# Performance work log

Measured on AMD Instinct MI355X. Metric: run time of the kernel, lower is better.

The kernel has to match this reference:

```python
import jax, jax.numpy as jnp
import numpy as np

N = 100000   # nodes
D = 128      # embedding_dim
E = 1600000  # edges
L = 3        # num_layers


def setup_inputs() -> dict:
    key = jax.random.key(0)
    ks = jax.random.split(key, 10)
    s = 1.0 / np.sqrt(D)
    def w(k, shape):
        return jax.random.uniform(k, shape, jnp.float32, -s, s)
    return {
        "x": jax.random.normal(ks[0], (N, D), jnp.float32),
        "edge_index": jax.random.randint(ks[1], (2, E), 0, N, jnp.int32),
        "Wp": w(ks[2], (L - 1, D, D)),   # project Linear weight (per layer)
        "bp": w(ks[3], (L - 1, D)),      # project Linear bias
        "Wl": w(ks[4], (L - 1, D, D)),   # lin_l (aggregated neighbors)
        "bl": w(ks[5], (L - 1, D)),
        "Wr": w(ks[6], (L - 1, D, D)),   # lin_r (root, no bias)
        "Wl_out": w(ks[7], (D, D)),
        "bl_out": w(ks[8], (D,)),
        "Wr_out": w(ks[9], (D, D)),
    }


def _sage(x, src, dst, inv_deg, Wl, bl, Wr, Wp=None, bp=None, normalize=False):
    # PyG SAGEConv: project applies to messages only; root term uses original x.
    h = jax.nn.relu(x @ Wp.T + bp) if Wp is not None else x
    agg = jax.ops.segment_sum(h[src], dst, num_segments=N) * inv_deg  # mean aggr
    out = agg @ Wl.T + bl + x @ Wr.T
    if normalize:
        out = out / jnp.maximum(
            jnp.linalg.norm(out, axis=-1, keepdims=True), 1e-12)
    return out


def reference(x, edge_index, Wp, bp, Wl, bl, Wr, Wl_out, bl_out, Wr_out):
    src, dst = edge_index[0], edge_index[1]
    deg = jax.ops.segment_sum(jnp.ones((src.shape[0],), x.dtype), dst,
                              num_segments=N)
    inv_deg = (1.0 / jnp.maximum(deg, 1.0))[:, None]  # isolated nodes -> 0 agg
    for i in range(L - 1):
        x = jax.nn.relu(
            _sage(x, src, dst, inv_deg, Wl[i], bl[i], Wr[i], Wp[i], bp[i],
                  normalize=True))
    return _sage(x, src, dst, inv_deg, Wl_out, bl_out, Wr_out)
```

## Files before the change

kernel.cpp:

```cpp
#include <hip/hip_runtime.h>
#include <math.h>

#define D 128

typedef short s8v __attribute__((ext_vector_type(8)));
typedef float f32x4 __attribute__((ext_vector_type(4)));
typedef unsigned short u16x8 __attribute__((ext_vector_type(8)));

__device__ __forceinline__ unsigned short f2bf(float f) {
  union { float f; unsigned u; } c; c.f = f;
  unsigned u = c.u;
  unsigned r = (u + 0x7fffu + ((u >> 16) & 1u)) >> 16;
  return (unsigned short)r;
}

__device__ __forceinline__ void gload_lds16(const void* g, void* l) {
  __builtin_amdgcn_global_load_lds((const __attribute__((address_space(1))) void*)g,
                                   (__attribute__((address_space(3))) void*)l, 16, 0, 0);
}

__global__ __launch_bounds__(256) void k_prep(const float* __restrict__ Wp,
                                              const float* __restrict__ Wl,
                                              const float* __restrict__ Wr,
                                              const float* __restrict__ Wlo,
                                              const float* __restrict__ Wro,
                                              unsigned short* __restrict__ Wb,
                                              const int* __restrict__ dst,
                                              int* __restrict__ bucketCnt, int E_) {
  int t = threadIdx.x;
  if (blockIdx.x < 128) {
    int i = blockIdx.x * 256 + t;
    const float* s;
    int off;
    if (i < 8192)       { s = Wp;  off = 0; }
    else if (i < 16384) { s = Wl;  off = 8192; }
    else if (i < 24576) { s = Wr;  off = 16384; }
    else if (i < 28672) { s = Wlo; off = 24576; }
    else                { s = Wro; off = 28672; }
    float4 a = ((const float4*)s)[i - off];
    ushort4 o;
    o.x = f2bf(a.x); o.y = f2bf(a.y); o.z = f2bf(a.z); o.w = f2bf(a.w);
    ((ushort4*)Wb)[i] = o;
  } else {
    __shared__ int hist[512];
    hist[t] = 0; hist[t + 256] = 0;
    __syncthreads();
    int base = (blockIdx.x - 128) * 4096;
#pragma unroll
    for (int i = 0; i < 16; i++) {
      int e = base + i * 256 + t;
      if (e < E_) atomicAdd(&hist[dst[e] >> 8], 1);
    }
    __syncthreads();
    int c = hist[t];       if (c) atomicAdd(&bucketCnt[t], c);
    c = hist[t + 256];     if (c) atomicAdd(&bucketCnt[t + 256], c);
  }
}

__global__ __launch_bounds__(512) void k_bucket_scan(const int* __restrict__ cnt,
                                                     int* __restrict__ base,
                                                     int* __restrict__ cursor,
                                                     int* __restrict__ row_start,
                                                     int n, int E_) {
  __shared__ int bs[512];
  int t = threadIdx.x;
  int orig = cnt[t];
  bs[t] = orig;
  __syncthreads();
  for (int off = 1; off < 512; off <<= 1) {
    int x = (t >= off) ? bs[t - off] : 0;
    __syncthreads();
    bs[t] += x;
    __syncthreads();
  }
  int ex = bs[t] - orig;
  base[t] = ex;
  cursor[t] = ex;
  if (t == 511) base[512] = bs[511];
  if (t == 0) row_start[n] = E_;
}

__global__ __launch_bounds__(1024) void k_partA(const int* __restrict__ src,
                                                const int* __restrict__ dst,
                                                int* __restrict__ cursor,
                                                unsigned* __restrict__ pairs, int E_) {
  __shared__ int hist[512];
  __shared__ int gbase[512];
  int t = threadIdx.x;
  int base = blockIdx.x * 16384;
  if (t < 512) hist[t] = 0;
  __syncthreads();
  unsigned p_[16];
  int k_[16];
#pragma unroll
  for (int i = 0; i < 16; i++) {
    int e = base + i * 1024 + t;
    if (e < E_) {
      int s = src[e], d = dst[e];
      p_[i] = ((unsigned)s << 8) | (unsigned)(d & 255);
      k_[i] = d >> 8;
      atomicAdd(&hist[k_[i]], 1);
    } else {
      k_[i] = -1;
    }
  }
  __syncthreads();
  if (t < 512) {
    int c = hist[t];
    gbase[t] = c ? atomicAdd(&cursor[t], c) : 0;
    hist[t] = 0;
  }
  __syncthreads();
#pragma unroll
  for (int i = 0; i < 16; i++) {
    if (k_[i] >= 0) {
      int r = atomicAdd(&hist[k_[i]], 1);
      pairs[gbase[k_[i]] + r] = p_[i];
    }
  }
}

__global__ __launch_bounds__(256) void k_partB(const unsigned* __restrict__ pairs,
                                               const int* __restrict__ bucketBase,
                                               int* __restrict__ row_start,
                                               int* __restrict__ csr, int n) {
  __shared__ int cnt[256];
  __shared__ int scn[256];
  int k = blockIdx.x, t = threadIdx.x;
  int node0 = k << 8;
  int pbeg = bucketBase[k], pend = bucketBase[k + 1];
  cnt[t] = 0;
  __syncthreads();
  for (int p = pbeg + t; p < pend; p += 256) atomicAdd(&cnt[pairs[p] & 255], 1);
  __syncthreads();
  int c = cnt[t];
  scn[t] = c;
  __syncthreads();
  for (int off = 1; off < 256; off <<= 1) {
    int x = (t >= off) ? scn[t - off] : 0;
    __syncthreads();
    scn[t] += x;
    __syncthreads();
  }
  int ex = scn[t] - c;
  int node = node0 + t;
  if (node < n) row_start[node] = pbeg + ex;
  __syncthreads();
  cnt[t] = pbeg + ex;
  __syncthreads();
  for (int p = pbeg + t; p < pend; p += 256) {
    unsigned pr = pairs[p];
    int slot = atomicAdd(&cnt[pr & 255], 1);
    csr[slot] = (int)(pr >> 8);
  }
}

__global__ __launch_bounds__(256) void k_aggregate(const unsigned short* __restrict__ h,
                                                   unsigned short* __restrict__ agg,
                                                   const int* __restrict__ row_start,
                                                   const int* __restrict__ csr, int n) {
  int node = (blockIdx.x * 256 + threadIdx.x) >> 4;
  int li = threadIdx.x & 15;
  if (node >= n) return;
  int rs0 = row_start[node];
  int dc = row_start[node + 1] - rs0;
  const int* ce = csr + rs0;
  const char* base = (const char*)h + li * 16;

  float accL[4], accH[4];
#pragma unroll
  for (int q = 0; q < 4; q++) { accL[q] = 0.f; accH[q] = 0.f; }

#define ACCR(v)                                                        \
  {                                                                    \
    unsigned dw[4] = {(v).x, (v).y, (v).z, (v).w};                     \
    _Pragma("unroll") for (int q = 0; q < 4; q++) {                    \
      accL[q] += __uint_as_float(dw[q] << 16);                         \
      accH[q] += __uint_as_float(dw[q] & 0xffff0000u);                 \
    }                                                                  \
  }

  int e = 0;
  bool more = (3 < dc);
  int s0 = 0, s1 = 0, s2 = 0, s3 = 0;
  if (more) { s0 = ce[0]; s1 = ce[1]; s2 = ce[2]; s3 = ce[3]; }
  while (more) {
    uint4 v0 = *(const uint4*)(base + (size_t)s0 * 256);
    uint4 v1 = *(const uint4*)(base + (size_t)s1 * 256);
    uint4 v2 = *(const uint4*)(base + (size_t)s2 * 256);
    uint4 v3 = *(const uint4*)(base + (size_t)s3 * 256);
    e += 4;
    more = (e + 3 < dc);
    if (more) { s0 = ce[e]; s1 = ce[e + 1]; s2 = ce[e + 2]; s3 = ce[e + 3]; }
    ACCR(v0); ACCR(v1); ACCR(v2); ACCR(v3);
  }
  if (e < dc)     { uint4 v = *(const uint4*)(base + (size_t)ce[e] * 256);     ACCR(v); }
  if (e + 1 < dc) { uint4 v = *(const uint4*)(base + (size_t)ce[e + 1] * 256); ACCR(v); }
  if (e + 2 < dc) { uint4 v = *(const uint4*)(base + (size_t)ce[e + 2] * 256); ACCR(v); }
#undef ACCR

  float iv = 1.0f / (float)(dc > 0 ? dc : 1);
  u16x8 o;
#pragma unroll
  for (int q = 0; q < 4; q++) {
    o[2 * q] = f2bf(accL[q] * iv);
    o[2 * q + 1] = f2bf(accH[q] * iv);
  }
  *(u16x8*)(agg + (size_t)node * D + li * 8) = o;
}

__device__ __forceinline__ int swz_chunk(int r, int c) { return (r << 4) + (c ^ (r & 7)); }

template <int CVT>
__global__ __launch_bounds__(512, 4) void k_gemm_proj(const void* __restrict__ Av,
                                                      const unsigned short* __restrict__ W,
                                                      const float* __restrict__ bias,
                                                      unsigned short* __restrict__ out,
                                                      unsigned short* __restrict__ xb_out,
                                                      int n) {
  __shared__ __align__(16) unsigned short Wlds[128 * 128];
  int t = threadIdx.x;
  int wv = t >> 6, l = t & 63, lg = l >> 4, ln = l & 15;
  int rb = blockIdx.x * 128 + wv * 16;
  int arow = rb + ln;
  if (arow >= n) arow = n - 1;

  s8v a[4];
  if (CVT) {
    const float* Af = (const float*)Av + (size_t)arow * D + lg * 8;
#pragma unroll
    for (int ks = 0; ks < 4; ++ks) {
      float4 f0 = *(const float4*)(Af + ks * 32);
      float4 f1 = *(const float4*)(Af + ks * 32 + 4);
      s8v av;
      av[0] = (short)f2bf(f0.x); av[1] = (short)f2bf(f0.y);
      av[2] = (short)f2bf(f0.z); av[3] = (short)f2bf(f0.w);
      av[4] = (short)f2bf(f1.x); av[5] = (short)f2bf(f1.y);
      av[6] = (short)f2bf(f1.z); av[7] = (short)f2bf(f1.w);
      a[ks] = av;
      if (xb_out) *(s8v*)(xb_out + (size_t)arow * D + lg * 8 + ks * 32) = av;
    }
  } else {
    const s8v* Ap = (const s8v*)((const unsigned short*)Av + (size_t)arow * D + lg * 8);
#pragma unroll
    for (int ks = 0; ks < 4; ++ks) a[ks] = Ap[ks * 4];
  }

#pragma unroll
  for (int i = 0; i < 4; ++i) {
    int idx = t + i * 512;
    int r = idx >> 4, k = idx & 15;
    int c = k ^ (r & 7);
    gload_lds16(W + r * 128 + c * 8, &Wlds[idx * 8]);
  }
  __syncthreads();

  f32x4 acc[8];
#pragma unroll
  for (int f = 0; f < 8; ++f) acc[f] = (f32x4){0.f, 0.f, 0.f, 0.f};
#pragma unroll
  for (int ks = 0; ks < 4; ++ks) {
#pragma unroll
    for (int f = 0; f < 8; ++f) {
      s8v b = *(const s8v*)&Wlds[swz_chunk(f * 16 + ln, ks * 4 + lg) * 8];
      acc[f] = __builtin_amdgcn_mfma_f32_16x16x32_bf16(a[ks], b, acc[f], 0, 0, 0);
    }
  }

#pragma unroll
  for (int r = 0; r < 4; ++r) {
    int gr = rb + 4 * lg + r;
    if (gr < n) {
#pragma unroll
      for (int f = 0; f < 8; ++f) {
        int c = f * 16 + ln;
        float v = acc[f][r] + bias[c];
        v = fmaxf(v, 0.f);
        out[(size_t)gr * D + c] = f2bf(v);
      }
    }
  }
}

template <int MODE>
__global__ __launch_bounds__(512, 4) void k_gemm_dual(const unsigned short* __restrict__ A1,
                                                      const unsigned short* __restrict__ W1,
                                                      const float* __restrict__ bias,
                                                      const unsigned short* __restrict__ A2,
                                                      const unsigned short* __restrict__ W2,
                                                      void* __restrict__ outv, int n) {
  __shared__ __align__(16) unsigned short Wlds[2 * 128 * 128];
  int t = threadIdx.x;
  int wv = t >> 6, l = t & 63, lg = l >> 4, ln = l & 15;
  int rb = blockIdx.x * 128 + wv * 16;
  int arow = rb + ln;
  if (arow >= n) arow = n - 1;
  const s8v* A1p = (const s8v*)(A1 + (size_t)arow * D + lg * 8);
  const s8v* A2p = (const s8v*)(A2 + (size_t)arow * D + lg * 8);
  s8v a1[4], a2[4];
#pragma unroll
  for (int ks = 0; ks < 4; ++ks) { a1[ks] = A1p[ks * 4]; a2[ks] = A2p[ks * 4]; }

#pragma unroll
  for (int i = 0; i < 8; ++i) {
    int idx = t + i * 512;
    int mat = idx >> 11;
    int rem = idx & 2047;
    int r = rem >> 4, k = rem & 15;
    int c = k ^ (r & 7);
    const unsigned short* src = (mat ? W2 : W1) + r * 128 + c * 8;
    gload_lds16(src, &Wlds[idx * 8]);
  }
  __syncthreads();

  f32x4 acc[8];
#pragma unroll
  for (int f = 0; f < 8; ++f) acc[f] = (f32x4){0.f, 0.f, 0.f, 0.f};

#pragma unroll
  for (int ks = 0; ks < 4; ++ks) {
#pragma unroll
    for (int f = 0; f < 8; ++f) {
      int ch = swz_chunk(f * 16 + ln, ks * 4 + lg) * 8;
      s8v b1 = *(const s8v*)&Wlds[ch];
      s8v b2 = *(const s8v*)&Wlds[16384 + ch];
      acc[f] = __builtin_amdgcn_mfma_f32_16x16x32_bf16(a1[ks], b1, acc[f], 0, 0, 0);
      acc[f] = __builtin_amdgcn_mfma_f32_16x16x32_bf16(a2[ks], b2, acc[f], 0, 0, 0);
    }
  }

#pragma unroll
  for (int r = 0; r < 4; ++r) {
    int gr = rb + 4 * lg + r;
    float v[8];
#pragma unroll
    for (int f = 0; f < 8; ++f) v[f] = acc[f][r] + bias[f * 16 + ln];
    if (MODE == 0) {
      float ss = 0.f;
#pragma unroll
      for (int f = 0; f < 8; ++f) ss += v[f] * v[f];
      ss += __shfl_xor(ss, 1);
      ss += __shfl_xor(ss, 2);
      ss += __shfl_xor(ss, 4);
      ss += __shfl_xor(ss, 8);
      float sc = 1.0f / fmaxf(sqrtf(ss), 1e-12f);
      if (gr < n) {
        unsigned short* out = (unsigned short*)outv;
#pragma unroll
        for (int f = 0; f < 8; ++f) {
          float o = fmaxf(v[f] * sc, 0.f);
          out[(size_t)gr * D + f * 16 + ln] = f2bf(o);
        }
      }
    } else {
      if (gr < n) {
        float* out = (float*)outv;
#pragma unroll
        for (int f = 0; f < 8; ++f) out[(size_t)gr * D + f * 16 + ln] = v[f];
      }
    }
  }
}

extern "C" void kernel_launch(void* const* d_in, const int* in_sizes, int n_in,
                              void* d_out, int out_size, void* d_ws, size_t ws_size,
                              hipStream_t stream) {
  const float* x   = (const float*)d_in[0];
  const int*   ei  = (const int*)d_in[1];
  const float* Wp  = (const float*)d_in[2];
  const float* bp  = (const float*)d_in[3];
  const float* Wl  = (const float*)d_in[4];
  const float* bl  = (const float*)d_in[5];
  const float* Wr  = (const float*)d_in[6];
  const float* Wlo = (const float*)d_in[7];
  const float* blo = (const float*)d_in[8];
  const float* Wro = (const float*)d_in[9];

  const int N = in_sizes[0] / D;
  const int E = in_sizes[1] / 2;
  const int* srcIdx = ei;
  const int* dstIdx = ei + E;

  const size_t ND = (size_t)N * D;

  unsigned short* xb   = (unsigned short*)d_ws;
  unsigned short* h    = xb + ND;
  unsigned short* aggB = h + ND;
  unsigned short* x2   = aggB + ND;
  unsigned short* Wb   = x2 + ND;
  int* row_start  = (int*)(Wb + 8 * 16384);
  int* bucketCnt  = row_start + N + 1;
  int* bucketBase = bucketCnt + 512;
  int* cursor     = bucketBase + 513;
  int* csr        = cursor + 512;

  unsigned* pairs = (unsigned*)aggB;

  unsigned short* Wpb0 = Wb;
  unsigned short* Wpb1 = Wb + 16384;
  unsigned short* Wlb0 = Wb + 2 * 16384;
  unsigned short* Wlb1 = Wb + 3 * 16384;
  unsigned short* Wrb0 = Wb + 4 * 16384;
  unsigned short* Wrb1 = Wb + 5 * 16384;
  unsigned short* Wlob = Wb + 6 * 16384;
  unsigned short* Wrob = Wb + 7 * 16384;

  unsigned short* x1 = (unsigned short*)d_out;

  int gG = (N + 127) / 128;
  int gAg = (N * 16 + 255) / 256;
  int KB = (N + 255) / 256;
  int gBC = (E + 4095) / 4096;
  int gA  = (E + 16383) / 16384;

  hipMemsetAsync(bucketCnt, 0, 512 * sizeof(int), stream);
  k_prep<<<128 + gBC, 256, 0, stream>>>(Wp, Wl, Wr, Wlo, Wro, Wb, dstIdx, bucketCnt, E);

  k_bucket_scan<<<1, 512, 0, stream>>>(bucketCnt, bucketBase, cursor, row_start, N, E);
  k_partA<<<gA, 1024, 0, stream>>>(srcIdx, dstIdx, cursor, pairs, E);
  k_partB<<<KB, 256, 0, stream>>>(pairs, bucketBase, row_start, csr, N);

  k_gemm_proj<1><<<gG, 512, 0, stream>>>(x, Wpb0, bp, h, xb, N);
  k_aggregate<<<gAg, 256, 0, stream>>>(h, aggB, row_start, csr, N);
  k_gemm_dual<0><<<gG, 512, 0, stream>>>(aggB, Wlb0, bl, xb, Wrb0, (void*)x1, N);

  k_gemm_proj<0><<<gG, 512, 0, stream>>>(x1, Wpb1, bp + D, h, nullptr, N);
  k_aggregate<<<gAg, 256, 0, stream>>>(h, aggB, row_start, csr, N);
  k_gemm_dual<0><<<gG, 512, 0, stream>>>(aggB, Wlb1, bl + D, x1, Wrb1, (void*)x2, N);

  k_aggregate<<<gAg, 256, 0, stream>>>(x2, aggB, row_start, csr, N);
  k_gemm_dual<1><<<gG, 512, 0, stream>>>(aggB, Wlob, blo, x2, Wrob, d_out, N);
}
```

Baseline: 333.7 us.

## Split bf16 feature matrices into 8 column slabs for cache-local gather aggregation

Intermediate bf16 activations (h, agg, xb, x1/x2) are stored as 8 slabs of 16 columns each (slab-major, node rows of 32 bytes) instead of row-major 256-byte rows. The aggregate kernel now assigns each block one slab and 128 nodes, with two threads per node, so the gather working set per slab (about 3.2 MB) can stay in L2/LLC while random neighbor rows are fetched. The GEMM kernels are updated to read and write the slabbed layout. In exchange each gather is only 16 bytes per thread, CSR indices are re-read once per slab, and the GEMM epilogue stores become more scattered.

```diff
diff --git a/kernel.cpp b/kernel.cpp
--- a/kernel.cpp
+++ b/kernel.cpp
@@ -18,6 +18,7 @@
   __builtin_amdgcn_global_load_lds((const __attribute__((address_space(1))) void*)g,
                                    (__attribute__((address_space(3))) void*)l, 16, 0, 0);
 }
+
 
 __global__ __launch_bounds__(256) void k_prep(const float* __restrict__ Wp,
                                               const float* __restrict__ Wl,
@@ -159,24 +160,28 @@
                                                    unsigned short* __restrict__ agg,
                                                    const int* __restrict__ row_start,
                                                    const int* __restrict__ csr, int n) {
-  int node = (blockIdx.x * 256 + threadIdx.x) >> 4;
-  int li = threadIdx.x & 15;
+  int s = blockIdx.x & 7;
+  int chunk = blockIdx.x >> 3;
+  int t = threadIdx.x;
+  int node = chunk * 128 + (t >> 1);
+  int li = t & 1;
   if (node >= n) return;
+  size_t n16 = (size_t)n * 16;
   int rs0 = row_start[node];
   int dc = row_start[node + 1] - rs0;
   const int* ce = csr + rs0;
-  const char* base = (const char*)h + li * 16;
-
-  float accL[4], accH[4];
-#pragma unroll
-  for (int q = 0; q < 4; q++) { accL[q] = 0.f; accH[q] = 0.f; }
+  const char* base = (const char*)(h + (size_t)s * n16) + li * 16;
+
+  float acc[8];
+#pragma unroll
+  for (int q = 0; q < 8; q++) acc[q] = 0.f;
 
 #define ACCR(v)                                                        \
   {                                                                    \
     unsigned dw[4] = {(v).x, (v).y, (v).z, (v).w};                     \
     _Pragma("unroll") for (int q = 0; q < 4; q++) {                    \
-      accL[q] += __uint_as_float(dw[q] << 16);                         \
-      accH[q] += __uint_as_float(dw[q] & 0xffff0000u);                 \
+      acc[2 * q] += __uint_as_float(dw[q] << 16);                      \
+      acc[2 * q + 1] += __uint_as_float(dw[q] & 0xffff0000u);          \
     }                                                                  \
   }
 
@@ -185,28 +190,25 @@
   int s0 = 0, s1 = 0, s2 = 0, s3 = 0;
   if (more) { s0 = ce[0]; s1 = ce[1]; s2 = ce[2]; s3 = ce[3]; }
   while (more) {
-    uint4 v0 = *(const uint4*)(base + (size_t)s0 * 256);
-    uint4 v1 = *(const uint4*)(base + (size_t)s1 * 256);
-    uint4 v2 = *(const uint4*)(base + (size_t)s2 * 256);
-    uint4 v3 = *(const uint4*)(base + (size_t)s3 * 256);
+    uint4 v0 = *(const uint4*)(base + (size_t)s0 * 32);
+    uint4 v1 = *(const uint4*)(base + (size_t)s1 * 32);
+    uint4 v2 = *(const uint4*)(base + (size_t)s2 * 32);
+    uint4 v3 = *(const uint4*)(base + (size_t)s3 * 32);
     e += 4;
     more = (e + 3 < dc);
     if (more) { s0 = ce[e]; s1 = ce[e + 1]; s2 = ce[e + 2]; s3 = ce[e + 3]; }
     ACCR(v0); ACCR(v1); ACCR(v2); ACCR(v3);
   }
-  if (e < dc)     { uint4 v = *(const uint4*)(base + (size_t)ce[e] * 256);     ACCR(v); }
-  if (e + 1 < dc) { uint4 v = *(const uint4*)(base + (size_t)ce[e + 1] * 256); ACCR(v); }
-  if (e + 2 < dc) { uint4 v = *(const uint4*)(base + (size_t)ce[e + 2] * 256); ACCR(v); }
+  if (e < dc)     { uint4 v = *(const uint4*)(base + (size_t)ce[e] * 32);     ACCR(v); }
+  if (e + 1 < dc) { uint4 v = *(const uint4*)(base + (size_t)ce[e + 1] * 32); ACCR(v); }
+  if (e + 2 < dc) { uint4 v = *(const uint4*)(base + (size_t)ce[e + 2] * 32); ACCR(v); }
 #undef ACCR
 
   float iv = 1.0f / (float)(dc > 0 ? dc : 1);
   u16x8 o;
 #pragma unroll
-  for (int q = 0; q < 4; q++) {
-    o[2 * q] = f2bf(accL[q] * iv);
-    o[2 * q + 1] = f2bf(accH[q] * iv);
-  }
-  *(u16x8*)(agg + (size_t)node * D + li * 8) = o;
+  for (int q = 0; q < 8; q++) o[q] = f2bf(acc[q] * iv);
+  *(u16x8*)(agg + (size_t)s * n16 + (size_t)node * 16 + li * 8) = o;
 }
 
 __device__ __forceinline__ int swz_chunk(int r, int c) { return (r << 4) + (c ^ (r & 7)); }
@@ -224,6 +226,7 @@
   int rb = blockIdx.x * 128 + wv * 16;
   int arow = rb + ln;
   if (arow >= n) arow = n - 1;
+  size_t n16 = (size_t)n * 16;
 
   s8v a[4];
   if (CVT) {
@@ -238,12 +241,18 @@
       av[4] = (short)f2bf(f1.x); av[5] = (short)f2bf(f1.y);
       av[6] = (short)f2bf(f1.z); av[7] = (short)f2bf(f1.w);
       a[ks] = av;
-      if (xb_out) *(s8v*)(xb_out + (size_t)arow * D + lg * 8 + ks * 32) = av;
+      if (xb_out) {
+        int c0 = ks * 32 + lg * 8;
+        *(s8v*)(xb_out + (size_t)(c0 >> 4) * n16 + (size_t)arow * 16 + (c0 & 15)) = av;
+      }
     }
   } else {
-    const s8v* Ap = (const s8v*)((const unsigned short*)Av + (size_t)arow * D + lg * 8);
-#pragma unroll
-    for (int ks = 0; ks < 4; ++ks) a[ks] = Ap[ks * 4];
+    const unsigned short* Ab = (const unsigned short*)Av;
+#pragma unroll
+    for (int ks = 0; ks < 4; ++ks) {
+      int c0 = ks * 32 + lg * 8;
+      a[ks] = *(const s8v*)(Ab + (size_t)(c0 >> 4) * n16 + (size_t)arow * 16 + (c0 & 15));
+    }
   }
 
 #pragma unroll
@@ -273,10 +282,9 @@
     if (gr < n) {
 #pragma unroll
       for (int f = 0; f < 8; ++f) {
-        int c = f * 16 + ln;
-        float v = acc[f][r] + bias[c];
+        float v = acc[f][r] + bias[f * 16 + ln];
         v = fmaxf(v, 0.f);
-        out[(size_t)gr * D + c] = f2bf(v);
+        out[(size_t)f * n16 + (size_t)gr * 16 + ln] = f2bf(v);
       }
     }
   }
@@ -295,11 +303,15 @@
   int rb = blockIdx.x * 128 + wv * 16;
   int arow = rb + ln;
   if (arow >= n) arow = n - 1;
-  const s8v* A1p = (const s8v*)(A1 + (size_t)arow * D + lg * 8);
-  const s8v* A2p = (const s8v*)(A2 + (size_t)arow * D + lg * 8);
+  size_t n16 = (size_t)n * 16;
   s8v a1[4], a2[4];
 #pragma unroll
-  for (int ks = 0; ks < 4; ++ks) { a1[ks] = A1p[ks * 4]; a2[ks] = A2p[ks * 4]; }
+  for (int ks = 0; ks < 4; ++ks) {
+    int c0 = ks * 32 + lg * 8;
+    size_t off = (size_t)(c0 >> 4) * n16 + (size_t)arow * 16 + (c0 & 15);
+    a1[ks] = *(const s8v*)(A1 + off);
+    a2[ks] = *(const s8v*)(A2 + off);
+  }
 
 #pragma unroll
   for (int i = 0; i < 8; ++i) {
@@ -349,7 +361,7 @@
 #pragma unroll
         for (int f = 0; f < 8; ++f) {
           float o = fmaxf(v[f] * sc, 0.f);
-          out[(size_t)gr * D + f * 16 + ln] = f2bf(o);
+          out[(size_t)f * n16 + (size_t)gr * 16 + ln] = f2bf(o);
         }
       }
     } else {
@@ -408,7 +420,7 @@
   unsigned short* x1 = (unsigned short*)d_out;
 
   int gG = (N + 127) / 128;
-  int gAg = (N * 16 + 255) / 256;
+  int gAg = ((N + 127) / 128) * 8;
   int KB = (N + 255) / 256;
   int gBC = (E + 4095) / 4096;
   int gA  = (E + 16383) / 16384;
```

Result: slower. 408.3 us (+22.3%).

## Fuse first projection GEMM with CSR partition-B into one heterogeneous launch

Applied to the files above, without the earlier changes.

The first-layer projection GEMM (fp32 input to bf16, with relu) and the CSR bucket finalisation (partB) now run as two block types inside a single 1024-thread kernel, so the two independent pieces of work can overlap on the GPU and one launch is dropped. The GEMM blocks now cover 256 rows each, using 16 waves. The partB blocks run with 1024 threads, but only 256 of them do the scan, so those blocks keep many threads idle. The larger block size and the shared LDS allocation may lower occupancy.

```diff
diff --git a/kernel.cpp b/kernel.cpp
--- a/kernel.cpp
+++ b/kernel.cpp
@@ -120,38 +120,108 @@
   }
 }
 
-__global__ __launch_bounds__(256) void k_partB(const unsigned* __restrict__ pairs,
-                                               const int* __restrict__ bucketBase,
-                                               int* __restrict__ row_start,
-                                               int* __restrict__ csr, int n) {
+__device__ __forceinline__ int swz_chunk(int r, int c) { return (r << 4) + (c ^ (r & 7)); }
+
+__global__ __launch_bounds__(1024, 4) void k_proj0B(const float* __restrict__ Av,
+                                                    const unsigned short* __restrict__ W,
+                                                    const float* __restrict__ bias,
+                                                    unsigned short* __restrict__ out,
+                                                    unsigned short* __restrict__ xb_out,
+                                                    const unsigned* __restrict__ pairs,
+                                                    const int* __restrict__ bucketBase,
+                                                    int* __restrict__ row_start,
+                                                    int* __restrict__ csr,
+                                                    int n, int nP) {
+  __shared__ __align__(16) unsigned short Wlds[128 * 128];
   __shared__ int cnt[256];
   __shared__ int scn[256];
-  int k = blockIdx.x, t = threadIdx.x;
-  int node0 = k << 8;
-  int pbeg = bucketBase[k], pend = bucketBase[k + 1];
-  cnt[t] = 0;
-  __syncthreads();
-  for (int p = pbeg + t; p < pend; p += 256) atomicAdd(&cnt[pairs[p] & 255], 1);
-  __syncthreads();
-  int c = cnt[t];
-  scn[t] = c;
-  __syncthreads();
-  for (int off = 1; off < 256; off <<= 1) {
-    int x = (t >= off) ? scn[t - off] : 0;
-    __syncthreads();
-    scn[t] += x;
-    __syncthreads();
-  }
-  int ex = scn[t] - c;
-  int node = node0 + t;
-  if (node < n) row_start[node] = pbeg + ex;
-  __syncthreads();
-  cnt[t] = pbeg + ex;
-  __syncthreads();
-  for (int p = pbeg + t; p < pend; p += 256) {
-    unsigned pr = pairs[p];
-    int slot = atomicAdd(&cnt[pr & 255], 1);
-    csr[slot] = (int)(pr >> 8);
+  int t = threadIdx.x;
+
+  if ((int)blockIdx.x < nP) {
+    int wv = t >> 6, l = t & 63, lg = l >> 4, ln = l & 15;
+    int rb = blockIdx.x * 256 + wv * 16;
+    int arow = rb + ln;
+    if (arow >= n) arow = n - 1;
+
+    s8v a[4];
+    const float* Af = Av + (size_t)arow * D + lg * 8;
+#pragma unroll
+    for (int ks = 0; ks < 4; ++ks) {
+      float4 f0 = *(const float4*)(Af + ks * 32);
+      float4 f1 = *(const float4*)(Af + ks * 32 + 4);
+      s8v av;
+      av[0] = (short)f2bf(f0.x); av[1] = (short)f2bf(f0.y);
+      av[2] = (short)f2bf(f0.z); av[3] = (short)f2bf(f0.w);
+      av[4] = (short)f2bf(f1.x); av[5] = (short)f2bf(f1.y);
+      av[6] = (short)f2bf(f1.z); av[7] = (short)f2bf(f1.w);
+      a[ks] = av;
+      *(s8v*)(xb_out + (size_t)arow * D + lg * 8 + ks * 32) = av;
+    }
+
+#pragma unroll
+    for (int i = 0; i < 2; ++i) {
+      int idx = t + i * 1024;
+      int r = idx >> 4, k = idx & 15;
+      int c = k ^ (r & 7);
+      gload_lds16(W + r * 128 + c * 8, &Wlds[idx * 8]);
+    }
+    __syncthreads();
+
+    f32x4 acc[8];
+#pragma unroll
+    for (int f = 0; f < 8; ++f) acc[f] = (f32x4){0.f, 0.f, 0.f, 0.f};
+#pragma unroll
+    for (int ks = 0; ks < 4; ++ks) {
+#pragma unroll
+      for (int f = 0; f < 8; ++f) {
+        s8v b = *(const s8v*)&Wlds[swz_chunk(f * 16 + ln, ks * 4 + lg) * 8];
+        acc[f] = __builtin_amdgcn_mfma_f32_16x16x32_bf16(a[ks], b, acc[f], 0, 0, 0);
+      }
+    }
+
+#pragma unroll
+    for (int r = 0; r < 4; ++r) {
+      int gr = rb + 4 * lg + r;
+      if (gr < n) {
+#pragma unroll
+        for (int f = 0; f < 8; ++f) {
+          int c = f * 16 + ln;
+          float v = acc[f][r] + bias[c];
+          v = fmaxf(v, 0.f);
+          out[(size_t)gr * D + c] = f2bf(v);
+        }
+      }
+    }
+  } else {
+    int k = blockIdx.x - nP;
+    int node0 = k << 8;
+    int pbeg = bucketBase[k], pend = bucketBase[k + 1];
+    if (t < 256) cnt[t] = 0;
+    __syncthreads();
+    for (int p = pbeg + t; p < pend; p += 1024) atomicAdd(&cnt[pairs[p] & 255], 1);
+    __syncthreads();
+    int c = 0;
+    if (t < 256) { c = cnt[t]; scn[t] = c; }
+    __syncthreads();
+    for (int off = 1; off < 256; off <<= 1) {
+      int xv = 0;
+      if (t < 256 && t >= off) xv = scn[t - off];
+      __syncthreads();
+      if (t < 256) scn[t] += xv;
+      __syncthreads();
+    }
+    if (t < 256) {
+      int ex = scn[t] - c;
+      int node = node0 + t;
+      if (node < n) row_start[node] = pbeg + ex;
+      cnt[t] = pbeg + ex;
+    }
+    __syncthreads();
+    for (int p = pbeg + t; p < pend; p += 1024) {
+      unsigned pr = pairs[p];
+      int slot = atomicAdd(&cnt[pr & 255], 1);
+      csr[slot] = (int)(pr >> 8);
+    }
   }
 }
 
@@ -209,14 +279,10 @@
   *(u16x8*)(agg + (size_t)node * D + li * 8) = o;
 }
 
-__device__ __forceinline__ int swz_chunk(int r, int c) { return (r << 4) + (c ^ (r & 7)); }
-
-template <int CVT>
-__global__ __launch_bounds__(512, 4) void k_gemm_proj(const void* __restrict__ Av,
+__global__ __launch_bounds__(512, 4) void k_gemm_proj(const unsigned short* __restrict__ A,
                                                       const unsigned short* __restrict__ W,
                                                       const float* __restrict__ bias,
                                                       unsigned short* __restrict__ out,
-                                                      unsigned short* __restrict__ xb_out,
                                                       int n) {
   __shared__ __align__(16) unsigned short Wlds[128 * 128];
   int t = threadIdx.x;
@@ -225,26 +291,10 @@
   int arow = rb + ln;
   if (arow >= n) arow = n - 1;
 
+  const s8v* Ap = (const s8v*)(A + (size_t)arow * D + lg * 8);
   s8v a[4];
-  if (CVT) {
-    const float* Af = (const float*)Av + (size_t)arow * D + lg * 8;
-#pragma unroll
-    for (int ks = 0; ks < 4; ++ks) {
-      float4 f0 = *(const float4*)(Af + ks * 32);
-      float4 f1 = *(const float4*)(Af + ks * 32 + 4);
-      s8v av;
-      av[0] = (short)f2bf(f0.x); av[1] = (short)f2bf(f0.y);
-      av[2] = (short)f2bf(f0.z); av[3] = (short)f2bf(f0.w);
-      av[4] = (short)f2bf(f1.x); av[5] = (short)f2bf(f1.y);
-      av[6] = (short)f2bf(f1.z); av[7] = (short)f2bf(f1.w);
-      a[ks] = av;
-      if (xb_out) *(s8v*)(xb_out + (size_t)arow * D + lg * 8 + ks * 32) = av;
-    }
-  } else {
-    const s8v* Ap = (const s8v*)((const unsigned short*)Av + (size_t)arow * D + lg * 8);
-#pragma unroll
-    for (int ks = 0; ks < 4; ++ks) a[ks] = Ap[ks * 4];
-  }
+#pragma unroll
+  for (int ks = 0; ks < 4; ++ks) a[ks] = Ap[ks * 4];
 
 #pragma unroll
   for (int i = 0; i < 4; ++i) {
@@ -407,9 +457,10 @@
 
   unsigned short* x1 = (unsigned short*)d_out;
 
-  int gG = (N + 127) / 128;
+  int gG  = (N + 127) / 128;
+  int gP  = (N + 255) / 256;
   int gAg = (N * 16 + 255) / 256;
-  int KB = (N + 255) / 256;
+  int KB  = (N + 255) / 256;
   int gBC = (E + 4095) / 4096;
   int gA  = (E + 16383) / 16384;
 
@@ -418,13 +469,14 @@
 
   k_bucket_scan<<<1, 512, 0, stream>>>(bucketCnt, bucketBase, cursor, row_start, N, E);
   k_partA<<<gA, 1024, 0, stream>>>(srcIdx, dstIdx, cursor, pairs, E);
-  k_partB<<<KB, 256, 0, stream>>>(pairs, bucketBase, row_start, csr, N);
-
-  k_gemm_proj<1><<<gG, 512, 0, stream>>>(x, Wpb0, bp, h, xb, N);
+
+  k_proj0B<<<gP + KB, 1024, 0, stream>>>(x, Wpb0, bp, h, xb,
+                                         pairs, bucketBase, row_start, csr, N, gP);
+
   k_aggregate<<<gAg, 256, 0, stream>>>(h, aggB, row_start, csr, N);
   k_gemm_dual<0><<<gG, 512, 0, stream>>>(aggB, Wlb0, bl, xb, Wrb0, (void*)x1, N);
 
-  k_gemm_proj<0><<<gG, 512, 0, stream>>>(x1, Wpb1, bp + D, h, nullptr, N);
+  k_gemm_proj<<<gG, 512, 0, stream>>>(x1, Wpb1, bp + D, h, N);
   k_aggregate<<<gAg, 256, 0, stream>>>(h, aggB, row_start, csr, N);
   k_gemm_dual<0><<<gG, 512, 0, stream>>>(aggB, Wlb1, bl + D, x1, Wrb1, (void*)x2, N);
 
```

Result: faster. 323.6 us (-3.0%).
